# Optimization experiments

Measured on AMD Instinct MI355X. Metric: run time of the kernel, lower is better.

## Reference

```python
import jax, jax.numpy as jnp
import numpy as np

N = 100000
E = 1600000
IN = 128
HID = 128
OUT = 64


def sage_conv(x, src, dst, deg_inv, W_l, b_l, W_r):
    # PyG SAGEConv (mean aggr): out = lin_l(mean_{j in N(i)} x_j) + lin_r(x_i)
    msgs = x[src]                                   # [E, F] gather
    agg = jax.ops.segment_sum(msgs, dst, num_segments=N)  # [N, F]
    agg = agg * deg_inv[:, None]                    # mean
    return agg @ W_l + b_l + x @ W_r


def setup_inputs() -> dict:
    key = jax.random.key(0)
    ks = jax.random.split(key, 9)
    x = jax.random.normal(ks[0], (N, IN), dtype=jnp.float32)
    edge_index = jax.random.randint(ks[1], (2, E), 0, N, dtype=jnp.int64)
    s = 1.0 / np.sqrt(IN)
    W1l = jax.random.uniform(ks[2], (IN, HID), jnp.float32, -s, s)
    b1 = jax.random.uniform(ks[3], (HID,), jnp.float32, -s, s)
    W1r = jax.random.uniform(ks[4], (IN, HID), jnp.float32, -s, s)
    s2 = 1.0 / np.sqrt(HID)
    W2l = jax.random.uniform(ks[5], (HID, HID), jnp.float32, -s2, s2)
    b2 = jax.random.uniform(ks[6], (HID,), jnp.float32, -s2, s2)
    W2r = jax.random.uniform(ks[7], (HID, HID), jnp.float32, -s2, s2)
    kl1, kl2 = jax.random.split(ks[8])
    Wlin = jax.random.uniform(kl1, (HID, OUT), jnp.float32, -s2, s2)
    blin = jax.random.uniform(kl2, (OUT,), jnp.float32, -s2, s2)
    return {"x": x, "edge_index": edge_index, "W1l": W1l, "b1": b1, "W1r": W1r,
            "W2l": W2l, "b2": b2, "W2r": W2r, "Wlin": Wlin, "blin": blin}


def reference(x, edge_index, W1l, b1, W1r, W2l, b2, W2r, Wlin, blin):
    src, dst = edge_index[0], edge_index[1]
    deg = jax.ops.segment_sum(jnp.ones((E,), jnp.float32), dst, num_segments=N)
    deg_inv = 1.0 / jnp.maximum(deg, 1.0)
    h = sage_conv(x, src, dst, deg_inv, W1l, b1, W1r)
    h = jax.nn.relu(h)
    # dropout: training=False -> identity
    h2 = sage_conv(h, src, dst, deg_inv, W2l, b2, W2r)
    h = jax.nn.relu(h + h2)
    return h @ Wlin + blin
```

## Files before the change

### kernel.cpp

```cpp
#include <hip/hip_runtime.h>
#include <hip/hip_bf16.h>
#include <cstdint>

#define NND 100000
#define NED 1600000
#define FIN 128
#define FOUT 64

#define NBLK 512
#define EPB (NED / NBLK)
#define NBUCK 256
#define BSH 9
#define BNODES 512
#define HTN (NBUCK * NBLK)

#define NSLICE 4
#define NPW 8
#define AGGB_BLK (NSLICE * (NND / (NPW * 4)))
#define EMAX 512

typedef __bf16 bf16x8 __attribute__((ext_vector_type(8)));
typedef float f32x4 __attribute__((ext_vector_type(4)));

static __device__ inline unsigned short f2bf(float f) {
    unsigned int u = __builtin_bit_cast(unsigned int, f);
    unsigned int r = (u + 0x7fffu + ((u >> 16) & 1u)) >> 16;
    return (unsigned short)r;
}
static __device__ inline float bflo(unsigned int v) {
    return __builtin_bit_cast(float, v << 16);
}
static __device__ inline float bfhi(unsigned int v) {
    return __builtin_bit_cast(float, v & 0xffff0000u);
}
static __device__ inline float bf1(unsigned short u) {
    return __builtin_bit_cast(float, (unsigned int)u << 16);
}

static __device__ inline void pack_one(const float* __restrict__ W,
                                       unsigned short* __restrict__ out,
                                       int NTtot, int c_local, int nt,
                                       int chunkOff, int ncols, int lane) {
    int k = c_local * 32 + (lane >> 4) * 8;
    int n = nt * 16 + (lane & 15);
    unsigned short t[8];
#pragma unroll
    for (int j = 0; j < 8; j++) t[j] = f2bf(W[(size_t)(k + j) * ncols + n]);
    uint4 u;
    u.x = t[0] | ((unsigned)t[1] << 16);
    u.y = t[2] | ((unsigned)t[3] << 16);
    u.z = t[4] | ((unsigned)t[5] << 16);
    u.w = t[6] | ((unsigned)t[7] << 16);
    *(uint4*)&out[((size_t)((c_local + chunkOff) * NTtot + nt) * 64 + lane) * 8] = u;
}

__global__ __launch_bounds__(256) void k_hist_cast(
        const int* __restrict__ dst, int* __restrict__ histT,
        const float* __restrict__ x, unsigned int* __restrict__ xb,
        const float* W1l, const float* W1r, const float* W2l,
        const float* W2r, const float* Wlin,
        unsigned short* p1, unsigned short* p2, unsigned short* ph) {
    __shared__ int hist[NBUCK];
    const int tid = threadIdx.x, blk = blockIdx.x;
    hist[tid] = 0;
    __syncthreads();
    const int e0 = blk * EPB, e1 = e0 + EPB;
    for (int i = e0 + tid; i < e1; i += 256)
        atomicAdd(&hist[dst[i] >> BSH], 1);
    __syncthreads();
    histT[tid * NBLK + blk] = hist[tid];
    if (blk < 144 && tid < 64) {
        int b = blk, lane = tid;
        if (b < 32)       pack_one(W1l, p1, 8, b >> 3, b & 7, 0, 128, lane);
        else if (b < 64)  { b -= 32; pack_one(W1r, p1, 8, b >> 3, b & 7, 4, 128, lane); }
        else if (b < 96)  { b -= 64; pack_one(W2l, p2, 8, b >> 3, b & 7, 0, 128, lane); }
        else if (b < 128) { b -= 96; pack_one(W2r, p2, 8, b >> 3, b & 7, 4, 128, lane); }
        else              { b -= 128; pack_one(Wlin, ph, 4, b >> 2, b & 3, 0, 64, lane); }
    }
    const int total = NND * 32;
    for (int j = blk * 256 + tid; j < total; j += NBLK * 256) {
        int sNode = j >> 3;
        int part = j & 7;
        int s = sNode / NND;
        int node = sNode - s * NND;
        float4 v = ((const float4*)x)[node * 32 + s * 8 + part];
        uint2 o;
        o.x = (unsigned)f2bf(v.x) | ((unsigned)f2bf(v.y) << 16);
        o.y = (unsigned)f2bf(v.z) | ((unsigned)f2bf(v.w) << 16);
        ((uint2*)xb)[j] = o;
    }
}

__global__ __launch_bounds__(1024) void g_scan1(const int* __restrict__ in,
                                                int* __restrict__ psum, int n) {
    __shared__ int red[1024];
    int tid = threadIdx.x;
    int i = blockIdx.x * 1024 + tid;
    red[tid] = (i < n) ? in[i] : 0;
    __syncthreads();
#pragma unroll
    for (int off = 512; off > 0; off >>= 1) {
        if (tid < off) red[tid] += red[tid + off];
        __syncthreads();
    }
    if (tid == 0) psum[blockIdx.x] = red[0];
}

__global__ __launch_bounds__(128) void g_scan2(int* __restrict__ psum, int nb) {
    int tid = threadIdx.x;
    int d = (tid < nb) ? psum[tid] : 0;
    int v = d;
#pragma unroll
    for (int off = 1; off < 64; off <<= 1) {
        int u = __shfl_up(v, off, 64);
        if ((tid & 63) >= off) v += u;
    }
    __shared__ int ws[2];
    if ((tid & 63) == 63) ws[tid >> 6] = v;
    __syncthreads();
    int base = (tid >= 64) ? ws[0] : 0;
    if (tid < nb) psum[tid] = base + v - d;
}

__global__ __launch_bounds__(1024) void g_scan3(const int* __restrict__ in,
                                                const int* __restrict__ psum,
                                                int* __restrict__ out, int n) {
    int tid = threadIdx.x;
    int i = blockIdx.x * 1024 + tid;
    int d = (i < n) ? in[i] : 0;
    int v = d;
#pragma unroll
    for (int off = 1; off < 64; off <<= 1) {
        int u = __shfl_up(v, off, 64);
        if ((tid & 63) >= off) v += u;
    }
    __shared__ int wsum[16];
    int wid = tid >> 6;
    if ((tid & 63) == 63) wsum[wid] = v;
    __syncthreads();
    if (tid < 16) {
        int w = wsum[tid];
#pragma unroll
        for (int off = 1; off < 16; off <<= 1) {
            int u = __shfl_up(w, off, 64);
            if (tid >= off) w += u;
        }
        wsum[tid] = w;
    }
    __syncthreads();
    int base = psum[blockIdx.x] + (wid ? wsum[wid - 1] : 0);
    if (i < n) out[i] = base + v - d;
}

__global__ __launch_bounds__(256) void k_scatter(const int* __restrict__ src,
                                                 const int* __restrict__ dst,
                                                 const int* __restrict__ sh,
                                                 uint2* __restrict__ eS) {
    __shared__ int cur[NBUCK];
    const int tid = threadIdx.x, blk = blockIdx.x;
    cur[tid] = sh[tid * NBLK + blk];
    __syncthreads();
    const int e0 = blk * EPB, e1 = e0 + EPB;
    for (int i = e0 + tid; i < e1; i += 256) {
        int d = dst[i];
        int pos = atomicAdd(&cur[d >> BSH], 1);
        eS[pos] = make_uint2((unsigned)src[i], (unsigned)(d & (BNODES - 1)));
    }
}

__global__ __launch_bounds__(1024) void k_bucket(const uint2* __restrict__ eS,
                                                 const int* __restrict__ sh,
                                                 int* __restrict__ csr,
                                                 int* __restrict__ offs,
                                                 float* __restrict__ dinv, int n) {
    __shared__ int cnt[BNODES];
    __shared__ int loc[BNODES];
    const int b = blockIdx.x, tid = threadIdx.x;
    const int base = sh[b * NBLK];
    const int end = (b == NBUCK - 1) ? NED : sh[(b + 1) * NBLK];
    if (tid < BNODES) cnt[tid] = 0;
    __syncthreads();
    for (int i = base + tid; i < end; i += 1024)
        atomicAdd(&cnt[eS[i].y], 1);
    __syncthreads();
    if (tid < BNODES) loc[tid] = cnt[tid];
    __syncthreads();
#pragma unroll
    for (int off = 1; off < BNODES; off <<= 1) {
        int v = 0;
        if (tid < BNODES && tid >= off) v = loc[tid - off];
        __syncthreads();
        if (tid < BNODES) loc[tid] += v;
        __syncthreads();
    }
    int node = b * BNODES + tid;
    int myExcl = 0;
    if (tid < BNODES) {
        myExcl = loc[tid] - cnt[tid];
        if (node < n) {
            offs[node] = base + myExcl;
            dinv[node] = 1.0f / fmaxf((float)cnt[tid], 1.0f);
        }
    }
    __syncthreads();
    if (tid < BNODES) cnt[tid] = base + myExcl;
    __syncthreads();
    for (int i = base + tid; i < end; i += 1024) {
        uint2 e = eS[i];
        int slot = atomicAdd(&cnt[e.y], 1);
        csr[slot] = (int)e.x;
    }
    if (b == 0 && tid == 0) offs[n] = NED;
}

#define ACC2(v) do { \
    acc.x += bflo((v).x); acc.y += bfhi((v).x); \
    acc.z += bflo((v).y); acc.w += bfhi((v).y); } while (0)

__global__ __launch_bounds__(256) void k_aggb(const unsigned short* __restrict__ featS,
                                              const int* __restrict__ offs,
                                              const int* __restrict__ csr,
                                              const float* __restrict__ dinv,
                                              unsigned short* __restrict__ outS, int n) {
    __shared__ int eids[4][EMAX];
    const int s = blockIdx.x & 3;
    const int wv = threadIdx.x >> 6;
    const int wslot = (blockIdx.x >> 2) * 4 + wv;
    const int lane = threadIdx.x & 63;
    const int g = lane >> 3;
    const int q = lane & 7;
    const uint2* fS = (const uint2*)featS + (size_t)s * n * 8;
    uint2* oS = (uint2*)outS + (size_t)s * n * 8;

    const int base = wslot * NPW;
    const int node = base + g;
    const bool valid = node < n;
    const int nc = valid ? node : n - 1;
    const int beg = offs[nc];
    const int end = offs[nc + 1];
    const int begW = __shfl(beg, 0);
    const int endW = __shfl(end, 63);
    const int lim = min(endW - begW, EMAX);
    for (int i = lane; i < lim; i += 64)
        eids[wv][i] = csr[begW + i];
    __syncthreads();

    f32x4 acc = (f32x4){0.f, 0.f, 0.f, 0.f};
    const int deg = valid ? (end - beg) : 0;
    const int lb = beg - begW;

    int j = 0;
    for (; j + 8 <= deg; j += 8) {
        int i0, i1, i2, i3, i4, i5, i6, i7;
        if (lb + j + 8 <= EMAX) {
            i0 = eids[wv][lb + j];     i1 = eids[wv][lb + j + 1];
            i2 = eids[wv][lb + j + 2]; i3 = eids[wv][lb + j + 3];
            i4 = eids[wv][lb + j + 4]; i5 = eids[wv][lb + j + 5];
            i6 = eids[wv][lb + j + 6]; i7 = eids[wv][lb + j + 7];
        } else {
            i0 = csr[beg + j];     i1 = csr[beg + j + 1];
            i2 = csr[beg + j + 2]; i3 = csr[beg + j + 3];
            i4 = csr[beg + j + 4]; i5 = csr[beg + j + 5];
            i6 = csr[beg + j + 6]; i7 = csr[beg + j + 7];
        }
        uint2 v0 = fS[(unsigned)i0 * 8u + q];
        uint2 v1 = fS[(unsigned)i1 * 8u + q];
        uint2 v2 = fS[(unsigned)i2 * 8u + q];
        uint2 v3 = fS[(unsigned)i3 * 8u + q];
        uint2 v4 = fS[(unsigned)i4 * 8u + q];
        uint2 v5 = fS[(unsigned)i5 * 8u + q];
        uint2 v6 = fS[(unsigned)i6 * 8u + q];
        uint2 v7 = fS[(unsigned)i7 * 8u + q];
        ACC2(v0); ACC2(v1); ACC2(v2); ACC2(v3);
        ACC2(v4); ACC2(v5); ACC2(v6); ACC2(v7);
    }
    {
        uint2 t0 = make_uint2(0u, 0u), t1 = t0, t2 = t0, t3 = t0;
        uint2 t4 = t0, t5 = t0, t6 = t0, t7 = t0;
#define TAIL(K, TV) do { \
        if (j + K < deg) { \
            int li = lb + j + K; \
            int id = (li < EMAX) ? eids[wv][li] : csr[begW + li]; \
            TV = fS[(unsigned)id * 8u + q]; \
        } } while (0)
        TAIL(0, t0); TAIL(1, t1); TAIL(2, t2); TAIL(3, t3);
        TAIL(4, t4); TAIL(5, t5); TAIL(6, t6); TAIL(7, t7);
#undef TAIL
        ACC2(t0); ACC2(t1); ACC2(t2); ACC2(t3);
        ACC2(t4); ACC2(t5); ACC2(t6); ACC2(t7);
    }

    if (valid) {
        float di = dinv[node];
        uint2 o;
        o.x = (unsigned)f2bf(acc.x * di) | ((unsigned)f2bf(acc.y * di) << 16);
        o.y = (unsigned)f2bf(acc.z * di) | ((unsigned)f2bf(acc.w * di) << 16);
        oS[(size_t)node * 8 + q] = o;
    }
}

template <int NT, int KCH, bool TWO, bool RELU, bool RESID, bool HEAD, bool OUTBF>
__global__ __launch_bounds__(256) void k_mfma(const unsigned short* __restrict__ P,
                                              const unsigned short* __restrict__ Q,
                                              const unsigned short* __restrict__ Wp,
                                              const float* __restrict__ bias,
                                              const unsigned short* __restrict__ resid,
                                              const unsigned short* __restrict__ Wp2,
                                              const float* __restrict__ bias2,
                                              void* __restrict__ outv, int n) {
    const int lane = threadIdx.x & 63;
    const int wave = threadIdx.x >> 6;
    const int quad = lane >> 4;
    const int row0 = blockIdx.x * 64 + wave * 16;
    int rowA = row0 + (lane & 15);
    if (rowA >= n) rowA = n - 1;

    f32x4 acc[NT];
#pragma unroll
    for (int t = 0; t < NT; t++) acc[t] = (f32x4){0.f, 0.f, 0.f, 0.f};

#pragma unroll
    for (int c = 0; c < KCH; c++) {
        const unsigned short* Abase = (TWO && c >= KCH / 2) ? Q : P;
        const int kk = (TWO ? (c & (KCH / 2 - 1)) : c) * 32 + quad * 8;
        bf16x8 a = *(const bf16x8*)&Abase[((size_t)(kk >> 5) * NND + rowA) * 32 + (kk & 31)];
#pragma unroll
        for (int t = 0; t < NT; t++) {
            bf16x8 b = *(const bf16x8*)&Wp[(size_t)((c * NT + t) * 64 + lane) * 8];
            acc[t] = __builtin_amdgcn_mfma_f32_16x16x32_bf16(a, b, acc[t], 0, 0, 0);
        }
    }

    const int col = lane & 15;
    if (!HEAD) {
#pragma unroll
        for (int t = 0; t < NT; t++) {
            float bv = bias[t * 16 + col];
#pragma unroll
            for (int r = 0; r < 4; r++) {
                int row = row0 + quad * 4 + r;
                if (row < n) {
                    float v = acc[t][r] + bv;
                    if (RESID) v += bf1(resid[((size_t)(t >> 1) * NND + row) * 32 + (t & 1) * 16 + col]);
                    if (RELU) v = fmaxf(v, 0.f);
                    if (OUTBF)
                        ((unsigned short*)outv)[((size_t)(t >> 1) * NND + row) * 32 + (t & 1) * 16 + col] = f2bf(v);
                    else
                        ((float*)outv)[(size_t)row * (NT * 16) + t * 16 + col] = v;
                }
            }
        }
    } else {
        __shared__ __align__(16) unsigned short sT[4][16 * 136];
#pragma unroll
        for (int t = 0; t < NT; t++) {
            float bv = bias[t * 16 + col];
#pragma unroll
            for (int r = 0; r < 4; r++) {
                int row = row0 + quad * 4 + r;
                int rr = row < n ? row : n - 1;
                float v = acc[t][r] + bv;
                if (RESID) v += bf1(resid[((size_t)(t >> 1) * NND + rr) * 32 + (t & 1) * 16 + col]);
                if (RELU) v = fmaxf(v, 0.f);
                sT[wave][(quad * 4 + r) * 136 + t * 16 + col] = f2bf(v);
            }
        }
        f32x4 hacc[4];
#pragma unroll
        for (int t = 0; t < 4; t++) hacc[t] = (f32x4){0.f, 0.f, 0.f, 0.f};
#pragma unroll
        for (int c = 0; c < 4; c++) {
            bf16x8 a = *(const bf16x8*)&sT[wave][(lane & 15) * 136 + c * 32 + quad * 8];
#pragma unroll
            for (int t = 0; t < 4; t++) {
                bf16x8 b = *(const bf16x8*)&Wp2[(size_t)((c * 4 + t) * 64 + lane) * 8];
                hacc[t] = __builtin_amdgcn_mfma_f32_16x16x32_bf16(a, b, hacc[t], 0, 0, 0);
            }
        }
#pragma unroll
        for (int t = 0; t < 4; t++) {
            float bv = bias2[t * 16 + col];
#pragma unroll
            for (int r = 0; r < 4; r++) {
                int row = row0 + quad * 4 + r;
                if (row < n)
                    ((float*)outv)[(size_t)row * 64 + t * 16 + col] = hacc[t][r] + bv;
            }
        }
    }
}

extern "C" void kernel_launch(void* const* d_in, const int* in_sizes, int n_in,
                              void* d_out, int out_size, void* d_ws, size_t ws_size,
                              hipStream_t stream) {
    const float* x    = (const float*)d_in[0];
    const int*   ei   = (const int*)d_in[1];
    const float* W1l  = (const float*)d_in[2];
    const float* b1   = (const float*)d_in[3];
    const float* W1r  = (const float*)d_in[4];
    const float* W2l  = (const float*)d_in[5];
    const float* b2   = (const float*)d_in[6];
    const float* W2r  = (const float*)d_in[7];
    const float* Wlin = (const float*)d_in[8];
    const float* blin = (const float*)d_in[9];
    float* out = (float*)d_out;

    const int N = NND, E = NED;
    const int* src = ei;
    const int* dst = ei + E;
    const int NB2 = HTN / 1024;

    char* w = (char*)d_ws;
    int*   histT  = (int*)w;               w += (size_t)HTN * 4;
    int*   sh     = (int*)w;               w += (size_t)HTN * 4;
    int*   psum   = (int*)w;               w += (size_t)NB2 * 4;
    int*   offs   = (int*)w;               w += (size_t)(N + 4) * 4;
    float* dinv   = (float*)w;             w += (size_t)N * 4;
    uint2* eS     = (uint2*)w;             w += (size_t)E * 8;
    int*   csr    = (int*)w;               w += (size_t)E * 4;
    unsigned short* p1  = (unsigned short*)w;  w += 256 * 128 * 2;
    unsigned short* p2  = (unsigned short*)w;  w += 256 * 128 * 2;
    unsigned short* ph  = (unsigned short*)w;  w += 128 * 64 * 2;
    unsigned short* xb  = (unsigned short*)w;  w += (size_t)N * 128 * 2;
    unsigned short* agg = (unsigned short*)w;  w += (size_t)N * 128 * 2;
    unsigned short* h1  = (unsigned short*)w;  w += (size_t)N * 128 * 2;

    k_hist_cast<<<NBLK, 256, 0, stream>>>(dst, histT, x, (unsigned int*)xb,
                                          W1l, W1r, W2l, W2r, Wlin, p1, p2, ph);
    g_scan1<<<NB2, 1024, 0, stream>>>(histT, psum, HTN);
    g_scan2<<<1, 128, 0, stream>>>(psum, NB2);
    g_scan3<<<NB2, 1024, 0, stream>>>(histT, psum, sh, HTN);
    k_scatter<<<NBLK, 256, 0, stream>>>(src, dst, sh, eS);
    k_bucket<<<NBUCK, 1024, 0, stream>>>(eS, sh, csr, offs, dinv, N);

    k_aggb<<<AGGB_BLK, 256, 0, stream>>>(xb, offs, csr, dinv, agg, N);
    k_mfma<8, 8, true, true, false, false, true><<<(N + 63) / 64, 256, 0, stream>>>(
        agg, xb, p1, b1, nullptr, nullptr, nullptr, h1, N);

    k_aggb<<<AGGB_BLK, 256, 0, stream>>>(h1, offs, csr, dinv, agg, N);
    k_mfma<8, 8, true, true, true, true, false><<<(N + 63) / 64, 256, 0, stream>>>(
        agg, h1, p2, b2, h1, ph, blin, out, N);
}
```

Measured before the change: 382.0 us.

## Use 8 feature slices for aggregation and stage MFMA weights in LDS

Features are re-laid out as 8 slices of 16 bf16 instead of 4 slices of 32. Each aggregation wave now handles 16 nodes with 4 lanes per node, so each gathered row segment is 32 bytes. The MFMA kernels become persistent grid-stride loops that copy the packed weight matrices into shared memory once per block instead of reading them from global memory per tile. The intent is better gather locality per slice and less repeated weight traffic. The trade-offs are narrower per-node gathers and a fixed grid size.

Result: slower. 415.0 us (+8.6%).

```diff
diff --git a/kernel.cpp b/kernel.cpp
--- a/kernel.cpp
+++ b/kernel.cpp
@@ -14,9 +14,9 @@
 #define BNODES 512
 #define HTN (NBUCK * NBLK)
 
-#define NSLICE 4
-#define NPW 8
-#define AGGB_BLK (NSLICE * (NND / (NPW * 4)))
+#define NSLICE 8
+#define NPWA 64
+#define AGGCHK ((NND + NPWA - 1) / NPWA)
 #define EMAX 512
 
 typedef __bf16 bf16x8 __attribute__((ext_vector_type(8)));
@@ -79,11 +79,11 @@
     }
     const int total = NND * 32;
     for (int j = blk * 256 + tid; j < total; j += NBLK * 256) {
-        int sNode = j >> 3;
-        int part = j & 7;
+        int sNode = j >> 2;
+        int part = j & 3;
         int s = sNode / NND;
         int node = sNode - s * NND;
-        float4 v = ((const float4*)x)[node * 32 + s * 8 + part];
+        float4 v = ((const float4*)x)[node * 32 + s * 4 + part];
         uint2 o;
         o.x = (unsigned)f2bf(v.x) | ((unsigned)f2bf(v.y) << 16);
         o.y = (unsigned)f2bf(v.z) | ((unsigned)f2bf(v.w) << 16);
@@ -223,32 +223,34 @@
                                               const float* __restrict__ dinv,
                                               unsigned short* __restrict__ outS, int n) {
     __shared__ int eids[4][EMAX];
-    const int s = blockIdx.x & 3;
+    const int s = blockIdx.x & 7;
+    const int chunk = blockIdx.x >> 3;
     const int wv = threadIdx.x >> 6;
-    const int wslot = (blockIdx.x >> 2) * 4 + wv;
     const int lane = threadIdx.x & 63;
-    const int g = lane >> 3;
-    const int q = lane & 7;
-    const uint2* fS = (const uint2*)featS + (size_t)s * n * 8;
-    uint2* oS = (uint2*)outS + (size_t)s * n * 8;
-
-    const int base = wslot * NPW;
-    const int node = base + g;
-    const bool valid = node < n;
-    const int nc = valid ? node : n - 1;
-    const int beg = offs[nc];
-    const int end = offs[nc + 1];
-    const int begW = __shfl(beg, 0);
-    const int endW = __shfl(end, 63);
+    const int g = lane >> 2;
+    const int q = lane & 3;
+    const uint2* fS = (const uint2*)featS + (size_t)s * n * 4;
+    uint2* oS = (uint2*)outS + (size_t)s * n * 4;
+
+    const int base = chunk * NPWA + wv * 16;
+    const int bW = base < n ? base : n;
+    const int eWn = base + 16 < n ? base + 16 : n;
+    const int begW = offs[bW];
+    const int endW = (bW < eWn) ? offs[eWn] : begW;
     const int lim = min(endW - begW, EMAX);
     for (int i = lane; i < lim; i += 64)
         eids[wv][i] = csr[begW + i];
     __syncthreads();
 
+    const int node = base + g;
+    const bool valid = node < n;
+    const int nd = valid ? node : n - 1;
+    const int beg = offs[nd];
+    const int end = valid ? offs[nd + 1] : beg;
+    const int deg = end - beg;
+    const int lb = beg - begW;
+
     f32x4 acc = (f32x4){0.f, 0.f, 0.f, 0.f};
-    const int deg = valid ? (end - beg) : 0;
-    const int lb = beg - begW;
-
     int j = 0;
     for (; j + 8 <= deg; j += 8) {
         int i0, i1, i2, i3, i4, i5, i6, i7;
@@ -263,14 +265,14 @@
             i4 = csr[beg + j + 4]; i5 = csr[beg + j + 5];
             i6 = csr[beg + j + 6]; i7 = csr[beg + j + 7];
         }
-        uint2 v0 = fS[(unsigned)i0 * 8u + q];
-        uint2 v1 = fS[(unsigned)i1 * 8u + q];
-        uint2 v2 = fS[(unsigned)i2 * 8u + q];
-        uint2 v3 = fS[(unsigned)i3 * 8u + q];
-        uint2 v4 = fS[(unsigned)i4 * 8u + q];
-        uint2 v5 = fS[(unsigned)i5 * 8u + q];
-        uint2 v6 = fS[(unsigned)i6 * 8u + q];
-        uint2 v7 = fS[(unsigned)i7 * 8u + q];
+        uint2 v0 = fS[(unsigned)i0 * 4u + q];
+        uint2 v1 = fS[(unsigned)i1 * 4u + q];
+        uint2 v2 = fS[(unsigned)i2 * 4u + q];
+        uint2 v3 = fS[(unsigned)i3 * 4u + q];
+        uint2 v4 = fS[(unsigned)i4 * 4u + q];
+        uint2 v5 = fS[(unsigned)i5 * 4u + q];
+        uint2 v6 = fS[(unsigned)i6 * 4u + q];
+        uint2 v7 = fS[(unsigned)i7 * 4u + q];
         ACC2(v0); ACC2(v1); ACC2(v2); ACC2(v3);
         ACC2(v4); ACC2(v5); ACC2(v6); ACC2(v7);
     }
@@ -280,8 +282,8 @@
 #define TAIL(K, TV) do { \
         if (j + K < deg) { \
             int li = lb + j + K; \
-            int id = (li < EMAX) ? eids[wv][li] : csr[begW + li]; \
-            TV = fS[(unsigned)id * 8u + q]; \
+            int id = (li < EMAX) ? eids[wv][li] : csr[beg + j + K]; \
+            TV = fS[(unsigned)id * 4u + q]; \
         } } while (0)
         TAIL(0, t0); TAIL(1, t1); TAIL(2, t2); TAIL(3, t3);
         TAIL(4, t4); TAIL(5, t5); TAIL(6, t6); TAIL(7, t7);
@@ -295,7 +297,7 @@
         uint2 o;
         o.x = (unsigned)f2bf(acc.x * di) | ((unsigned)f2bf(acc.y * di) << 16);
         o.y = (unsigned)f2bf(acc.z * di) | ((unsigned)f2bf(acc.w * di) << 16);
-        oS[(size_t)node * 8 + q] = o;
+        oS[(size_t)node * 4 + q] = o;
     }
 }
 
@@ -307,84 +309,99 @@
                                               const unsigned short* __restrict__ resid,
                                               const unsigned short* __restrict__ Wp2,
                                               const float* __restrict__ bias2,
-                                              void* __restrict__ outv, int n) {
-    const int lane = threadIdx.x & 63;
-    const int wave = threadIdx.x >> 6;
+                                              void* __restrict__ outv, int n, int ntiles) {
+    __shared__ __align__(16) unsigned short sB[KCH * NT * 64 * 8];
+    __shared__ __align__(16) unsigned short sB2[HEAD ? 4 * 4 * 64 * 8 : 8];
+    __shared__ __align__(16) unsigned short sT[HEAD ? 4 * 16 * 136 : 8];
+
+    const int tid = threadIdx.x;
+    for (int i = tid; i < KCH * NT * 64; i += 256)
+        *(uint4*)&sB[(size_t)i * 8] = *(const uint4*)&Wp[(size_t)i * 8];
+    if constexpr (HEAD) {
+        for (int i = tid; i < 4 * 4 * 64; i += 256)
+            *(uint4*)&sB2[(size_t)i * 8] = *(const uint4*)&Wp2[(size_t)i * 8];
+    }
+    __syncthreads();
+
+    const int lane = tid & 63;
+    const int wave = tid >> 6;
     const int quad = lane >> 4;
-    const int row0 = blockIdx.x * 64 + wave * 16;
-    int rowA = row0 + (lane & 15);
-    if (rowA >= n) rowA = n - 1;
-
-    f32x4 acc[NT];
-#pragma unroll
-    for (int t = 0; t < NT; t++) acc[t] = (f32x4){0.f, 0.f, 0.f, 0.f};
-
-#pragma unroll
-    for (int c = 0; c < KCH; c++) {
-        const unsigned short* Abase = (TWO && c >= KCH / 2) ? Q : P;
-        const int kk = (TWO ? (c & (KCH / 2 - 1)) : c) * 32 + quad * 8;
-        bf16x8 a = *(const bf16x8*)&Abase[((size_t)(kk >> 5) * NND + rowA) * 32 + (kk & 31)];
-#pragma unroll
-        for (int t = 0; t < NT; t++) {
-            bf16x8 b = *(const bf16x8*)&Wp[(size_t)((c * NT + t) * 64 + lane) * 8];
-            acc[t] = __builtin_amdgcn_mfma_f32_16x16x32_bf16(a, b, acc[t], 0, 0, 0);
+    const int col = lane & 15;
+
+    for (int tile = blockIdx.x; tile < ntiles; tile += gridDim.x) {
+        const int row0 = tile * 64 + wave * 16;
+        int rowA = row0 + col;
+        if (rowA >= n) rowA = n - 1;
+
+        f32x4 acc[NT];
+#pragma unroll
+        for (int t = 0; t < NT; t++) acc[t] = (f32x4){0.f, 0.f, 0.f, 0.f};
+
+#pragma unroll
+        for (int c = 0; c < KCH; c++) {
+            const unsigned short* Abase = (TWO && c >= KCH / 2) ? Q : P;
+            const int kk = (TWO ? (c & (KCH / 2 - 1)) : c) * 32 + quad * 8;
+            bf16x8 a = *(const bf16x8*)&Abase[((size_t)(kk >> 4) * NND + rowA) * 16 + (kk & 15)];
+#pragma unroll
+            for (int t = 0; t < NT; t++) {
+                bf16x8 b = *(const bf16x8*)&sB[(size_t)((c * NT + t) * 64 + lane) * 8];
+                acc[t] = __builtin_amdgcn_mfma_f32_16x16x32_bf16(a, b, acc[t], 0, 0, 0);
+            }
         }
-    }
-
-    const int col = lane & 15;
-    if (!HEAD) {
-#pragma unroll
-        for (int t = 0; t < NT; t++) {
-            float bv = bias[t * 16 + col];
-#pragma unroll
-            for (int r = 0; r < 4; r++) {
-                int row = row0 + quad * 4 + r;
-                if (row < n) {
-                    float v = acc[t][r] + bv;
-                    if (RESID) v += bf1(resid[((size_t)(t >> 1) * NND + row) * 32 + (t & 1) * 16 + col]);
-                    if (RELU) v = fmaxf(v, 0.f);
-                    if (OUTBF)
-                        ((unsigned short*)outv)[((size_t)(t >> 1) * NND + row) * 32 + (t & 1) * 16 + col] = f2bf(v);
-                    else
-                        ((float*)outv)[(size_t)row * (NT * 16) + t * 16 + col] = v;
+
+        if (!HEAD) {
+#pragma unroll
+            for (int t = 0; t < NT; t++) {
+                float bv = bias[t * 16 + col];
+#pragma unroll
+                for (int r = 0; r < 4; r++) {
+                    int row = row0 + quad * 4 + r;
+                    if (row < n) {
+                        float v = acc[t][r] + bv;
+                        if (RESID) v += bf1(resid[((size_t)t * NND + row) * 16 + col]);
+                        if (RELU) v = fmaxf(v, 0.f);
+                        if (OUTBF)
+                            ((unsigned short*)outv)[((size_t)t * NND + row) * 16 + col] = f2bf(v);
+                        else
+                            ((float*)outv)[(size_t)row * (NT * 16) + t * 16 + col] = v;
+                    }
                 }
             }
-        }
-    } else {
-        __shared__ __align__(16) unsigned short sT[4][16 * 136];
-#pragma unroll
-        for (int t = 0; t < NT; t++) {
-            float bv = bias[t * 16 + col];
-#pragma unroll
-            for (int r = 0; r < 4; r++) {
-                int row = row0 + quad * 4 + r;
-                int rr = row < n ? row : n - 1;
-                float v = acc[t][r] + bv;
-                if (RESID) v += bf1(resid[((size_t)(t >> 1) * NND + rr) * 32 + (t & 1) * 16 + col]);
-                if (RELU) v = fmaxf(v, 0.f);
-                sT[wave][(quad * 4 + r) * 136 + t * 16 + col] = f2bf(v);
+        } else {
+#pragma unroll
+            for (int t = 0; t < NT; t++) {
+                float bv = bias[t * 16 + col];
+#pragma unroll
+                for (int r = 0; r < 4; r++) {
+                    int row = row0 + quad * 4 + r;
+                    int rr = row < n ? row : n - 1;
+                    float v = acc[t][r] + bv;
+                    if (RESID) v += bf1(resid[((size_t)t * NND + rr) * 16 + col]);
+                    if (RELU) v = fmaxf(v, 0.f);
+                    sT[(size_t)wave * (16 * 136) + (quad * 4 + r) * 136 + t * 16 + col] = f2bf(v);
+                }
             }
-        }
-        f32x4 hacc[4];
-#pragma unroll
-        for (int t = 0; t < 4; t++) hacc[t] = (f32x4){0.f, 0.f, 0.f, 0.f};
-#pragma unroll
-        for (int c = 0; c < 4; c++) {
-            bf16x8 a = *(const bf16x8*)&sT[wave][(lane & 15) * 136 + c * 32 + quad * 8];
+            f32x4 hacc[4];
+#pragma unroll
+            for (int t = 0; t < 4; t++) hacc[t] = (f32x4){0.f, 0.f, 0.f, 0.f};
+#pragma unroll
+            for (int c = 0; c < 4; c++) {
+                bf16x8 a = *(const bf16x8*)&sT[(size_t)wave * (16 * 136) + (lane & 15) * 136 + c * 32 + quad * 8];
+#pragma unroll
+                for (int t = 0; t < 4; t++) {
+                    bf16x8 b = *(const bf16x8*)&sB2[(size_t)((c * 4 + t) * 64 + lane) * 8];
+                    hacc[t] = __builtin_amdgcn_mfma_f32_16x16x32_bf16(a, b, hacc[t], 0, 0, 0);
+                }
+            }
 #pragma unroll
             for (int t = 0; t < 4; t++) {
-                bf16x8 b = *(const bf16x8*)&Wp2[(size_t)((c * 4 + t) * 64 + lane) * 8];
-                hacc[t] = __builtin_amdgcn_mfma_f32_16x16x32_bf16(a, b, hacc[t], 0, 0, 0);
-            }
-        }
-#pragma unroll
-        for (int t = 0; t < 4; t++) {
-            float bv = bias2[t * 16 + col];
-#pragma unroll
-            for (int r = 0; r < 4; r++) {
-                int row = row0 + quad * 4 + r;
-                if (row < n)
-                    ((float*)outv)[(size_t)row * 64 + t * 16 + col] = hacc[t][r] + bv;
+                float bv = bias2[t * 16 + col];
+#pragma unroll
+                for (int r = 0; r < 4; r++) {
+                    int row = row0 + quad * 4 + r;
+                    if (row < n)
+                        ((float*)outv)[(size_t)row * 64 + t * 16 + col] = hacc[t][r] + bv;
+                }
             }
         }
     }
@@ -409,6 +426,7 @@
     const int* src = ei;
     const int* dst = ei + E;
     const int NB2 = HTN / 1024;
+    const int ntiles = (N + 63) / 64;
 
     char* w = (char*)d_ws;
     int*   histT  = (int*)w;               w += (size_t)HTN * 4;
@@ -433,11 +451,11 @@
     k_scatter<<<NBLK, 256, 0, stream>>>(src, dst, sh, eS);
     k_bucket<<<NBUCK, 1024, 0, stream>>>(eS, sh, csr, offs, dinv, N);
 
-    k_aggb<<<AGGB_BLK, 256, 0, stream>>>(xb, offs, csr, dinv, agg, N);
-    k_mfma<8, 8, true, true, false, false, true><<<(N + 63) / 64, 256, 0, stream>>>(
-        agg, xb, p1, b1, nullptr, nullptr, nullptr, h1, N);
-
-    k_aggb<<<AGGB_BLK, 256, 0, stream>>>(h1, offs, csr, dinv, agg, N);
-    k_mfma<8, 8, true, true, true, true, false><<<(N + 63) / 64, 256, 0, stream>>>(
-        agg, h1, p2, b2, h1, ph, blin, out, N);
-}
+    k_aggb<<<AGGCHK * 8, 256, 0, stream>>>(xb, offs, csr, dinv, agg, N);
+    k_mfma<8, 8, true, true, false, false, true><<<512, 256, 0, stream>>>(
+        agg, xb, p1, b1, nullptr, nullptr, nullptr, h1, N, ntiles);
+
+    k_aggb<<<AGGCHK * 8, 256, 0, stream>>>(h1, offs, csr, dinv, agg, N);
+    k_mfma<8, 8, true, true, true, true, false><<<256, 256, 0, stream>>>(
+        agg, h1, p2, b2, h1, ph, blin, out, N, ntiles);
+}
```

## Replace two-level bucket sort CSR build with direct global-atomic degree count and fill

Applied to the files above, without the earlier changes.

The CSR construction changes from a bucketed two-pass counting sort (per-block histograms, scan, scatter into an intermediate edge buffer, per-bucket local sort) to a direct approach. Per-node degrees are counted with global atomics, scanned into offsets, and source ids are placed into the CSR slot with global atomicAdd on a per-node cursor. This drops the intermediate 8-byte edge buffer and one kernel, at the cost of scattered global atomics with contention on node counters. Neighbor order within a node becomes nondeterministic. The aggregation tail's index fallback is also adjusted.

Result: slower. 541.3 us (+41.7%).

```diff
diff --git a/kernel.cpp b/kernel.cpp
--- a/kernel.cpp
+++ b/kernel.cpp
@@ -8,11 +8,6 @@
 #define FOUT 64
 
 #define NBLK 512
-#define EPB (NED / NBLK)
-#define NBUCK 256
-#define BSH 9
-#define BNODES 512
-#define HTN (NBUCK * NBLK)
 
 #define NSLICE 4
 #define NPW 8
@@ -55,20 +50,14 @@
 }
 
 __global__ __launch_bounds__(256) void k_hist_cast(
-        const int* __restrict__ dst, int* __restrict__ histT,
+        const int* __restrict__ dst, int* __restrict__ deg,
         const float* __restrict__ x, unsigned int* __restrict__ xb,
         const float* W1l, const float* W1r, const float* W2l,
         const float* W2r, const float* Wlin,
         unsigned short* p1, unsigned short* p2, unsigned short* ph) {
-    __shared__ int hist[NBUCK];
     const int tid = threadIdx.x, blk = blockIdx.x;
-    hist[tid] = 0;
-    __syncthreads();
-    const int e0 = blk * EPB, e1 = e0 + EPB;
-    for (int i = e0 + tid; i < e1; i += 256)
-        atomicAdd(&hist[dst[i] >> BSH], 1);
-    __syncthreads();
-    histT[tid * NBLK + blk] = hist[tid];
+    for (int i = blk * 256 + tid; i < NED; i += NBLK * 256)
+        atomicAdd(&deg[dst[i]], 1);
     if (blk < 144 && tid < 64) {
         int b = blk, lane = tid;
         if (b < 32)       pack_one(W1l, p1, 8, b >> 3, b & 7, 0, 128, lane);
@@ -122,12 +111,14 @@
     if (tid < nb) psum[tid] = base + v - d;
 }
 
-__global__ __launch_bounds__(1024) void g_scan3(const int* __restrict__ in,
-                                                const int* __restrict__ psum,
-                                                int* __restrict__ out, int n) {
+__global__ __launch_bounds__(1024) void k_scan3b(const int* __restrict__ deg,
+                                                 const int* __restrict__ psum,
+                                                 int* __restrict__ offs,
+                                                 int* __restrict__ cur,
+                                                 float* __restrict__ dinv, int n) {
     int tid = threadIdx.x;
     int i = blockIdx.x * 1024 + tid;
-    int d = (i < n) ? in[i] : 0;
+    int d = (i < n) ? deg[i] : 0;
     int v = d;
 #pragma unroll
     for (int off = 1; off < 64; off <<= 1) {
@@ -149,68 +140,24 @@
     }
     __syncthreads();
     int base = psum[blockIdx.x] + (wid ? wsum[wid - 1] : 0);
-    if (i < n) out[i] = base + v - d;
-}
-
-__global__ __launch_bounds__(256) void k_scatter(const int* __restrict__ src,
-                                                 const int* __restrict__ dst,
-                                                 const int* __restrict__ sh,
-                                                 uint2* __restrict__ eS) {
-    __shared__ int cur[NBUCK];
-    const int tid = threadIdx.x, blk = blockIdx.x;
-    cur[tid] = sh[tid * NBLK + blk];
-    __syncthreads();
-    const int e0 = blk * EPB, e1 = e0 + EPB;
-    for (int i = e0 + tid; i < e1; i += 256) {
+    if (i < n) {
+        int ex = base + v - d;
+        offs[i] = ex;
+        cur[i] = ex;
+        dinv[i] = 1.0f / fmaxf((float)d, 1.0f);
+        if (i == n - 1) offs[n] = ex + d;
+    }
+}
+
+__global__ __launch_bounds__(256) void k_fill(const int* __restrict__ src,
+                                              const int* __restrict__ dst,
+                                              int* __restrict__ cur,
+                                              int* __restrict__ csr) {
+    for (int i = blockIdx.x * 256 + threadIdx.x; i < NED; i += NBLK * 256) {
         int d = dst[i];
-        int pos = atomicAdd(&cur[d >> BSH], 1);
-        eS[pos] = make_uint2((unsigned)src[i], (unsigned)(d & (BNODES - 1)));
-    }
-}
-
-__global__ __launch_bounds__(1024) void k_bucket(const uint2* __restrict__ eS,
-                                                 const int* __restrict__ sh,
-                                                 int* __restrict__ csr,
-                                                 int* __restrict__ offs,
-                                                 float* __restrict__ dinv, int n) {
-    __shared__ int cnt[BNODES];
-    __shared__ int loc[BNODES];
-    const int b = blockIdx.x, tid = threadIdx.x;
-    const int base = sh[b * NBLK];
-    const int end = (b == NBUCK - 1) ? NED : sh[(b + 1) * NBLK];
-    if (tid < BNODES) cnt[tid] = 0;
-    __syncthreads();
-    for (int i = base + tid; i < end; i += 1024)
-        atomicAdd(&cnt[eS[i].y], 1);
-    __syncthreads();
-    if (tid < BNODES) loc[tid] = cnt[tid];
-    __syncthreads();
-#pragma unroll
-    for (int off = 1; off < BNODES; off <<= 1) {
-        int v = 0;
-        if (tid < BNODES && tid >= off) v = loc[tid - off];
-        __syncthreads();
-        if (tid < BNODES) loc[tid] += v;
-        __syncthreads();
-    }
-    int node = b * BNODES + tid;
-    int myExcl = 0;
-    if (tid < BNODES) {
-        myExcl = loc[tid] - cnt[tid];
-        if (node < n) {
-            offs[node] = base + myExcl;
-            dinv[node] = 1.0f / fmaxf((float)cnt[tid], 1.0f);
-        }
-    }
-    __syncthreads();
-    if (tid < BNODES) cnt[tid] = base + myExcl;
-    __syncthreads();
-    for (int i = base + tid; i < end; i += 1024) {
-        uint2 e = eS[i];
-        int slot = atomicAdd(&cnt[e.y], 1);
-        csr[slot] = (int)e.x;
-    }
-    if (b == 0 && tid == 0) offs[n] = NED;
+        int pos = atomicAdd(&cur[d], 1);
+        csr[pos] = src[i];
+    }
 }
 
 #define ACC2(v) do { \
@@ -280,7 +227,7 @@
 #define TAIL(K, TV) do { \
         if (j + K < deg) { \
             int li = lb + j + K; \
-            int id = (li < EMAX) ? eids[wv][li] : csr[begW + li]; \
+            int id = (li < EMAX) ? eids[wv][li] : csr[beg + j + K]; \
             TV = fS[(unsigned)id * 8u + q]; \
         } } while (0)
         TAIL(0, t0); TAIL(1, t1); TAIL(2, t2); TAIL(3, t3);
@@ -408,15 +355,14 @@
     const int N = NND, E = NED;
     const int* src = ei;
     const int* dst = ei + E;
-    const int NB2 = HTN / 1024;
+    const int NBS = (N + 1023) / 1024;
 
     char* w = (char*)d_ws;
-    int*   histT  = (int*)w;               w += (size_t)HTN * 4;
-    int*   sh     = (int*)w;               w += (size_t)HTN * 4;
-    int*   psum   = (int*)w;               w += (size_t)NB2 * 4;
+    int*   deg    = (int*)w;               w += (size_t)N * 4;
     int*   offs   = (int*)w;               w += (size_t)(N + 4) * 4;
+    int*   cur    = (int*)w;               w += (size_t)N * 4;
+    int*   psum   = (int*)w;               w += 128 * 4;
     float* dinv   = (float*)w;             w += (size_t)N * 4;
-    uint2* eS     = (uint2*)w;             w += (size_t)E * 8;
     int*   csr    = (int*)w;               w += (size_t)E * 4;
     unsigned short* p1  = (unsigned short*)w;  w += 256 * 128 * 2;
     unsigned short* p2  = (unsigned short*)w;  w += 256 * 128 * 2;
@@ -425,13 +371,13 @@
     unsigned short* agg = (unsigned short*)w;  w += (size_t)N * 128 * 2;
     unsigned short* h1  = (unsigned short*)w;  w += (size_t)N * 128 * 2;
 
-    k_hist_cast<<<NBLK, 256, 0, stream>>>(dst, histT, x, (unsigned int*)xb,
+    hipMemsetAsync(deg, 0, (size_t)N * 4, stream);
+    k_hist_cast<<<NBLK, 256, 0, stream>>>(dst, deg, x, (unsigned int*)xb,
                                           W1l, W1r, W2l, W2r, Wlin, p1, p2, ph);
-    g_scan1<<<NB2, 1024, 0, stream>>>(histT, psum, HTN);
-    g_scan2<<<1, 128, 0, stream>>>(psum, NB2);
-    g_scan3<<<NB2, 1024, 0, stream>>>(histT, psum, sh, HTN);
-    k_scatter<<<NBLK, 256, 0, stream>>>(src, dst, sh, eS);
-    k_bucket<<<NBUCK, 1024, 0, stream>>>(eS, sh, csr, offs, dinv, N);
+    g_scan1<<<NBS, 1024, 0, stream>>>(deg, psum, N);
+    g_scan2<<<1, 128, 0, stream>>>(psum, NBS);
+    k_scan3b<<<NBS, 1024, 0, stream>>>(deg, psum, offs, cur, dinv, N);
+    k_fill<<<NBLK, 256, 0, stream>>>(src, dst, cur, csr);
 
     k_aggb<<<AGGB_BLK, 256, 0, stream>>>(xb, offs, csr, dinv, agg, N);
     k_mfma<8, 8, true, true, false, false, true><<<(N + 63) / 64, 256, 0, stream>>>(
```
